# Kernel optimization log

Measured on AMD Instinct MI355X. Metric: run time of the kernel, lower is better.

## Reference

```python
import jax, jax.numpy as jnp
import numpy as np

B, T, C = 4, 2048, 1024
H = 16
HD = C // H


def setup_inputs() -> dict:
    key = jax.random.key(0)
    k1, k2, k3 = jax.random.split(key, 3)
    x = jax.random.normal(k1, (B, T, C), dtype=jnp.float32)
    w_qkv = jax.random.normal(k2, (C, 3 * C), dtype=jnp.float32) * (C ** -0.5)
    w_proj = jax.random.normal(k3, (C, C), dtype=jnp.float32) * (C ** -0.5)
    b_proj = jnp.zeros((C,), dtype=jnp.float32)
    return {"x": x, "w_qkv": w_qkv, "w_proj": w_proj, "b_proj": b_proj}


def reference(x, w_qkv, w_proj, b_proj):
    Bd, Td, Cd = x.shape
    scale = HD ** -0.5
    qkv = x @ w_qkv  # [B,T,3C]
    q, k, v = jnp.split(qkv, 3, axis=-1)
    # [B,H,T,HD]
    q = q.reshape(Bd, Td, H, HD).transpose(0, 2, 1, 3)
    k = k.reshape(Bd, Td, H, HD).transpose(0, 2, 1, 3)
    v = v.reshape(Bd, Td, H, HD).transpose(0, 2, 1, 3)
    att = jnp.einsum('bhqd,bhkd->bhqk', q, k) * scale
    causal = jnp.triu(jnp.ones((Td, Td), dtype=bool), k=1)
    att = jnp.where(causal, -jnp.inf, att)
    att = jax.nn.softmax(att, axis=-1)
    y = jnp.einsum('bhqk,bhkd->bhqd', att, v)
    y = y.transpose(0, 2, 1, 3).reshape(Bd, Td, Cd)
    return y @ w_proj + b_proj
```

## Files before the change

### kernel.cpp

```cpp
#include <hip/hip_runtime.h>

typedef unsigned short u16;
typedef __attribute__((ext_vector_type(8))) short short8;
typedef __attribute__((ext_vector_type(4))) short short4v;
typedef __attribute__((ext_vector_type(4))) float floatx4;
typedef __attribute__((ext_vector_type(4))) unsigned short ushort4v;

#define B_ 4
#define T_ 2048
#define C_ 1024
#define H_ 16
#define HD_ 64

static __device__ __forceinline__ u16 f2bf(float f) {
  union { float f; unsigned int i; } c; c.f = f;
  unsigned int u = c.i;
  return (u16)((u + 0x7FFFu + ((u >> 16) & 1u)) >> 16);
}
static __device__ __forceinline__ unsigned pk2(float lo, float hi) {
  union { float f; unsigned u; } a, b; a.f = hi; b.f = lo;
  return __builtin_amdgcn_perm(a.u, b.u, 0x07060302u);
}

static __device__ __forceinline__ void gload16(const u16* g, u16* l) {
  __builtin_amdgcn_global_load_lds(
      (const __attribute__((address_space(1))) unsigned int*)(g),
      (__attribute__((address_space(3))) unsigned int*)(l), 16, 0, 0);
}

__global__ __launch_bounds__(256) void prep_k(const float* __restrict__ x,
                                              const float* __restrict__ w_qkv,
                                              const float* __restrict__ w_proj,
                                              u16* __restrict__ xbf,
                                              u16* __restrict__ wqkvT,
                                              u16* __restrict__ wprojT) {
  const int bid = blockIdx.x;
  if (bid < 8192) {
    const int i = bid * 256 + threadIdx.x;
    const float4 f = ((const float4*)x)[i];
    ushort4v o;
    o.x = f2bf(f.x); o.y = f2bf(f.y); o.z = f2bf(f.z); o.w = f2bf(f.w);
    *(ushort4v*)(xbf + (size_t)i * 4) = o;
    return;
  }
  __shared__ u16 tile[32][33];
  const float* in;
  u16* out;
  int R, Cc, tb;
  if (bid < 11264) {
    in = w_qkv; out = wqkvT; R = C_; Cc = 3 * C_; tb = bid - 8192;
  } else {
    in = w_proj; out = wprojT; R = C_; Cc = C_; tb = bid - 11264;
  }
  const int tpr = Cc / 32;
  const int bx = (tb % tpr) * 32;
  const int by = (tb / tpr) * 32;
  const int tx = threadIdx.x & 31;
  const int ty = threadIdx.x >> 5;
  #pragma unroll
  for (int i = ty; i < 32; i += 8)
    tile[i][tx] = f2bf(in[(size_t)(by + i) * Cc + bx + tx]);
  __syncthreads();
  #pragma unroll
  for (int i = ty; i < 32; i += 8)
    out[(size_t)(bx + i) * R + by + tx] = tile[tx][i];
}

__global__ __launch_bounds__(256) void vtrans_k(const u16* __restrict__ qkv,
                                                u16* __restrict__ vt) {
  __shared__ u16 tile[64][74];
  const int tt = blockIdx.x;
  const int bh = blockIdx.y;
  const int b = bh >> 4, h = bh & 15;
  const int tid = threadIdx.x;
  const u16* src = qkv + ((size_t)b * T_ + tt * 64) * (3 * C_) + 2 * C_ + h * HD_;
  #pragma unroll
  for (int ss = tid; ss < 512; ss += 256) {
    const int row = ss >> 3, c8 = (ss & 7) * 8;
    *(short8*)(&tile[row][c8]) = *(const short8*)(src + (size_t)row * (3 * C_) + c8);
  }
  __syncthreads();
  u16* dst = vt + (size_t)bh * HD_ * T_ + tt * 64;
  #pragma unroll
  for (int ss = tid; ss < 512; ss += 256) {
    const int tc = (ss & 7) * 8, d = ss >> 3;
    short8 o;
    #pragma unroll
    for (int j = 0; j < 8; j++) o[j] = (short)tile[tc + j][d];
    *(short8*)(dst + (size_t)d * T_ + tc) = o;
  }
}

template <int MODE>
__global__ __launch_bounds__(256) void gemm_bt(const u16* __restrict__ A,
                                               const u16* __restrict__ Bt,
                                               u16* __restrict__ outb,
                                               float* __restrict__ outf,
                                               const float* __restrict__ bias,
                                               int M, int N, int K) {
  __shared__ __align__(16) u16 As[2][128 * 32];
  __shared__ __align__(16) u16 Bs[2][128 * 32];
  const int bid = blockIdx.x;
  const int s = bid >> 3;
  const int tM = ((bid & 7) * 8 + (s & 7)) * 128;
  const int tN = (s >> 3) * 128;
  const int tid = threadIdx.x;
  const int wave = tid >> 6;
  const int lane = tid & 63;
  const int lr = lane & 15;
  const int quad = lane >> 4;
  const int wm = (wave >> 1) * 64;
  const int wn = (wave & 1) * 64;

  const int srow = lane >> 2;
  const int skofs = ((lane & 3) ^ ((lane >> 3) & 3)) * 8;

  const floatx4 zf = {0.f, 0.f, 0.f, 0.f};
  floatx4 acc[4][4];
  #pragma unroll
  for (int i = 0; i < 4; i++)
    #pragma unroll
    for (int j = 0; j < 4; j++) acc[i][j] = zf;

  const int csw = (lr >> 1) & 3;

  for (int k0 = 0; k0 < K; k0 += 64) {
    __syncthreads();
    #pragma unroll
    for (int half = 0; half < 2; half++) {
      const int kk = k0 + half * 32;
      #pragma unroll
      for (int j = 0; j < 2; j++) {
        const int seg = wave * 2 + j;
        const int row = seg * 16 + srow;
        gload16(A + (size_t)(tM + row) * K + kk + skofs, &As[half][seg * 512]);
        gload16(Bt + (size_t)(tN + row) * K + kk + skofs, &Bs[half][seg * 512]);
      }
    }
    __syncthreads();

    #pragma unroll
    for (int half = 0; half < 2; half++) {
      short8 af[4], bfr[4];
      #pragma unroll
      for (int mt = 0; mt < 4; mt++)
        af[mt] = *(const short8*)(&As[half][(wm + mt * 16 + lr) * 32 + ((quad ^ csw) * 8)]);
      #pragma unroll
      for (int nt = 0; nt < 4; nt++)
        bfr[nt] = *(const short8*)(&Bs[half][(wn + nt * 16 + lr) * 32 + ((quad ^ csw) * 8)]);
      #pragma unroll
      for (int mt = 0; mt < 4; mt++)
        #pragma unroll
        for (int nt = 0; nt < 4; nt++)
          acc[mt][nt] = __builtin_amdgcn_mfma_f32_16x16x32_bf16(af[mt], bfr[nt],
                                                                acc[mt][nt], 0, 0, 0);
    }
  }

  #pragma unroll
  for (int mt = 0; mt < 4; mt++) {
    const int m0 = tM + wm + mt * 16 + quad * 4;
    #pragma unroll
    for (int nt = 0; nt < 4; nt++) {
      const int n = tN + wn + nt * 16 + lr;
      #pragma unroll
      for (int r = 0; r < 4; r++) {
        const float v = acc[mt][nt][r];
        const size_t m = (size_t)(m0 + r);
        if (MODE == 2) __builtin_nontemporal_store(v + bias[n], &outf[m * N + n]);
        else           outb[m * N + n] = f2bf(v);
      }
    }
  }
}

__global__ __launch_bounds__(256, 4) void attn_k(const u16* __restrict__ qkv,
                                                 const u16* __restrict__ vt,
                                                 u16* __restrict__ y) {
  __shared__ __align__(16) u16 Ks[64 * 64];
  __shared__ __align__(16) u16 Vs[64 * 64];
  const int bid = blockIdx.x;
  const int s = bid >> 3;
  const int qp = s >> 3;
  const int bh = ((s & 7) << 3) | (bid & 7);
  const int b = bh >> 4, h = bh & 15;
  const int tid = threadIdx.x;
  const int wave = tid >> 6;
  const int lane = tid & 63;
  const int lr = lane & 15;
  const int quad = lane >> 4;
  const int qtA = qp, qtB = 31 - qp;

  const int srow = lane >> 3;
  const int skofs = ((lane & 7) ^ ((lane >> 3) & 7)) * 8;
  const int gsw = lr & 7;

  const size_t RS = 3 * C_;
  const u16* qcol = qkv + (size_t)b * T_ * RS + h * HD_;
  const u16* kcol = qcol + C_;

  const size_t qrA = (size_t)(qtA * 64 + wave * 16 + lr) * RS;
  const size_t qrB = (size_t)(qtB * 64 + wave * 16 + lr) * RS;
  const short8 aq0A = *(const short8*)(qcol + qrA + quad * 8);
  const short8 aq1A = *(const short8*)(qcol + qrA + 32 + quad * 8);
  const short8 aq0B = *(const short8*)(qcol + qrB + quad * 8);
  const short8 aq1B = *(const short8*)(qcol + qrB + 32 + quad * 8);

  const floatx4 zf = {0.f, 0.f, 0.f, 0.f};
  const float C1 = 0.125f * 1.44269504f;
  const float C2 = -16.0f * 1.44269504f;
  const short8 vones = {16256, 16256, 16256, 16256, 16256, 16256, 16256, 16256};

  floatx4 accA[4], accB[4];
  floatx4 accSA = zf, accSB = zf;
  #pragma unroll
  for (int i = 0; i < 4; i++) { accA[i] = zf; accB[i] = zf; }

  for (int kt = 0; kt <= qtB; kt++) {
    const bool doA = (kt <= qtA);
    const bool diagA = (kt == qtA), diagB = (kt == qtB);
    __syncthreads();
    #pragma unroll
    for (int j = 0; j < 2; j++) {
      const int seg = wave * 2 + j;
      const int row = seg * 8 + srow;
      gload16(kcol + (size_t)(kt * 64 + row) * RS + skofs, &Ks[seg * 512]);
      gload16(vt + ((size_t)bh * HD_ + row) * T_ + kt * 64 + skofs, &Vs[seg * 512]);
    }
    __syncthreads();

    float peA[4][4], peB[4][4];
    #pragma unroll
    for (int nt = 0; nt < 4; nt++) {
      const short8 bk0 =
          *(const short8*)(&Ks[(nt * 16 + lr) * 64 + ((quad ^ gsw) * 8)]);
      const short8 bk1 =
          *(const short8*)(&Ks[(nt * 16 + lr) * 64 + (((quad + 4) ^ gsw) * 8)]);
      {
        floatx4 st = __builtin_amdgcn_mfma_f32_16x16x32_bf16(
            bk1, aq1B,
            __builtin_amdgcn_mfma_f32_16x16x32_bf16(bk0, aq0B, zf, 0, 0, 0),
            0, 0, 0);
        #pragma unroll
        for (int r = 0; r < 4; r++) {
          float pe = __builtin_amdgcn_exp2f(fmaf(st[r], C1, C2));
          if (diagB && (nt * 16 + quad * 4 + r > wave * 16 + lr)) pe = 0.f;
          peB[nt][r] = pe;
        }
      }
      if (doA) {
        floatx4 st = __builtin_amdgcn_mfma_f32_16x16x32_bf16(
            bk1, aq1A,
            __builtin_amdgcn_mfma_f32_16x16x32_bf16(bk0, aq0A, zf, 0, 0, 0),
            0, 0, 0);
        #pragma unroll
        for (int r = 0; r < 4; r++) {
          float pe = __builtin_amdgcn_exp2f(fmaf(st[r], C1, C2));
          if (diagA && (nt * 16 + quad * 4 + r > wave * 16 + lr)) pe = 0.f;
          peA[nt][r] = pe;
        }
      }
    }

    short8 pB[2], pA[2];
    #pragma unroll
    for (int h2 = 0; h2 < 2; h2++) {
      union { unsigned u[4]; short8 s8; } w;
      w.u[0] = pk2(peB[2 * h2][0], peB[2 * h2][1]);
      w.u[1] = pk2(peB[2 * h2][2], peB[2 * h2][3]);
      w.u[2] = pk2(peB[2 * h2 + 1][0], peB[2 * h2 + 1][1]);
      w.u[3] = pk2(peB[2 * h2 + 1][2], peB[2 * h2 + 1][3]);
      pB[h2] = w.s8;
    }
    if (doA) {
      #pragma unroll
      for (int h2 = 0; h2 < 2; h2++) {
        union { unsigned u[4]; short8 s8; } w;
        w.u[0] = pk2(peA[2 * h2][0], peA[2 * h2][1]);
        w.u[1] = pk2(peA[2 * h2][2], peA[2 * h2][3]);
        w.u[2] = pk2(peA[2 * h2 + 1][0], peA[2 * h2 + 1][1]);
        w.u[3] = pk2(peA[2 * h2 + 1][2], peA[2 * h2 + 1][3]);
        pA[h2] = w.s8;
      }
    }

    #pragma unroll
    for (int h2 = 0; h2 < 2; h2++) {
      accSB = __builtin_amdgcn_mfma_f32_16x16x32_bf16(vones, pB[h2], accSB, 0, 0, 0);
      if (doA)
        accSA = __builtin_amdgcn_mfma_f32_16x16x32_bf16(vones, pA[h2], accSA, 0, 0, 0);
      #pragma unroll
      for (int dt = 0; dt < 4; dt++) {
        const int base = (dt * 16 + lr) * 64;
        const int cl = h2 * 4 + (quad >> 1);
        const int off_lo = ((cl ^ gsw) * 8) + (quad & 1) * 4;
        const int off_hi = (((cl + 2) ^ gsw) * 8) + (quad & 1) * 4;
        const short4v vlo = *(const short4v*)(&Vs[base + off_lo]);
        const short4v vhi = *(const short4v*)(&Vs[base + off_hi]);
        const short8 av = __builtin_shufflevector(vlo, vhi, 0, 1, 2, 3, 4, 5, 6, 7);
        accB[dt] = __builtin_amdgcn_mfma_f32_16x16x32_bf16(av, pB[h2], accB[dt], 0, 0, 0);
        if (doA)
          accA[dt] = __builtin_amdgcn_mfma_f32_16x16x32_bf16(av, pA[h2], accA[dt], 0, 0, 0);
      }
    }
  }

  #pragma unroll
  for (int ph = 0; ph < 2; ph++) {
    const int qt = ph ? qtB : qtA;
    const floatx4* acc = ph ? accB : accA;
    const float inv = 1.f / (ph ? accSB[0] : accSA[0]);
    const int qg = qt * 64 + wave * 16 + lr;
    u16* yrow = y + ((size_t)(b * T_ + qg)) * C_ + h * HD_;
    #pragma unroll
    for (int dt = 0; dt < 4; dt++) {
      ushort4v o;
      #pragma unroll
      for (int r = 0; r < 4; r++) o[r] = f2bf(acc[dt][r] * inv);
      *(ushort4v*)(yrow + dt * 16 + quad * 4) = o;
    }
  }
}

extern "C" void kernel_launch(void* const* d_in, const int* in_sizes, int n_in,
                              void* d_out, int out_size, void* d_ws, size_t ws_size,
                              hipStream_t stream) {
  const float* x      = (const float*)d_in[0];
  const float* w_qkv  = (const float*)d_in[1];
  const float* w_proj = (const float*)d_in[2];
  const float* b_proj = (const float*)d_in[3];
  float* out = (float*)d_out;

  u16* ws = (u16*)d_ws;
  const size_t SZ = (size_t)B_ * T_ * C_;
  u16* xbf    = ws;
  u16* wqkvT  = xbf + SZ;
  u16* wprojT = wqkvT + (size_t)3 * C_ * C_;
  u16* qkvw   = wprojT + (size_t)C_ * C_;
  u16* vtw    = qkvw + 3 * SZ;
  u16* yw     = xbf;

  prep_k<<<12288, 256, 0, stream>>>(x, w_qkv, w_proj, xbf, wqkvT, wprojT);
  gemm_bt<1><<<1536, 256, 0, stream>>>(
      xbf, wqkvT, qkvw, nullptr, nullptr, B_ * T_, 3 * C_, C_);
  vtrans_k<<<dim3(T_ / 64, B_ * H_), 256, 0, stream>>>(qkvw, vtw);
  attn_k<<<1024, 256, 0, stream>>>(qkvw, vtw, yw);
  gemm_bt<2><<<512, 256, 0, stream>>>(
      yw, wprojT, nullptr, out, b_proj, B_ * T_, C_, C_);
}
```

Before: 246.0 us.

## Fuse V transpose into QKV GEMM epilogue via LDS staging

Removes the separate vtrans_k kernel. Output tiles of the QKV GEMM that fall in the V region are now transposed through shared memory and written straight into the [B,H,HD,T] layout. This saves one launch and a full read and write of V from global memory. In exchange, those V blocks pay extra epilogue syncs and LDS traffic, and the As/Bs buffers are merged into one LDS array so it can be reused.

```diff
diff --git a/kernel.cpp b/kernel.cpp
--- a/kernel.cpp
+++ b/kernel.cpp
@@ -20,6 +20,9 @@
 static __device__ __forceinline__ unsigned pk2(float lo, float hi) {
   union { float f; unsigned u; } a, b; a.f = hi; b.f = lo;
   return __builtin_amdgcn_perm(a.u, b.u, 0x07060302u);
+}
+static __device__ __forceinline__ unsigned pk2r(float lo, float hi) {
+  return (unsigned)f2bf(lo) | ((unsigned)f2bf(hi) << 16);
 }
 
 static __device__ __forceinline__ void gload16(const u16* g, u16* l) {
@@ -66,40 +69,15 @@
     out[(size_t)(bx + i) * R + by + tx] = tile[tx][i];
 }
 
-__global__ __launch_bounds__(256) void vtrans_k(const u16* __restrict__ qkv,
-                                                u16* __restrict__ vt) {
-  __shared__ u16 tile[64][74];
-  const int tt = blockIdx.x;
-  const int bh = blockIdx.y;
-  const int b = bh >> 4, h = bh & 15;
-  const int tid = threadIdx.x;
-  const u16* src = qkv + ((size_t)b * T_ + tt * 64) * (3 * C_) + 2 * C_ + h * HD_;
-  #pragma unroll
-  for (int ss = tid; ss < 512; ss += 256) {
-    const int row = ss >> 3, c8 = (ss & 7) * 8;
-    *(short8*)(&tile[row][c8]) = *(const short8*)(src + (size_t)row * (3 * C_) + c8);
-  }
-  __syncthreads();
-  u16* dst = vt + (size_t)bh * HD_ * T_ + tt * 64;
-  #pragma unroll
-  for (int ss = tid; ss < 512; ss += 256) {
-    const int tc = (ss & 7) * 8, d = ss >> 3;
-    short8 o;
-    #pragma unroll
-    for (int j = 0; j < 8; j++) o[j] = (short)tile[tc + j][d];
-    *(short8*)(dst + (size_t)d * T_ + tc) = o;
-  }
-}
-
 template <int MODE>
 __global__ __launch_bounds__(256) void gemm_bt(const u16* __restrict__ A,
                                                const u16* __restrict__ Bt,
                                                u16* __restrict__ outb,
+                                               u16* __restrict__ outv,
                                                float* __restrict__ outf,
                                                const float* __restrict__ bias,
                                                int M, int N, int K) {
-  __shared__ __align__(16) u16 As[2][128 * 32];
-  __shared__ __align__(16) u16 Bs[2][128 * 32];
+  __shared__ __align__(16) u16 lds[16384];
   const int bid = blockIdx.x;
   const int s = bid >> 3;
   const int tM = ((bid & 7) * 8 + (s & 7)) * 128;
@@ -133,8 +111,8 @@
       for (int j = 0; j < 2; j++) {
         const int seg = wave * 2 + j;
         const int row = seg * 16 + srow;
-        gload16(A + (size_t)(tM + row) * K + kk + skofs, &As[half][seg * 512]);
-        gload16(Bt + (size_t)(tN + row) * K + kk + skofs, &Bs[half][seg * 512]);
+        gload16(A + (size_t)(tM + row) * K + kk + skofs, &lds[half * 4096 + seg * 512]);
+        gload16(Bt + (size_t)(tN + row) * K + kk + skofs, &lds[8192 + half * 4096 + seg * 512]);
       }
     }
     __syncthreads();
@@ -144,10 +122,10 @@
       short8 af[4], bfr[4];
       #pragma unroll
       for (int mt = 0; mt < 4; mt++)
-        af[mt] = *(const short8*)(&As[half][(wm + mt * 16 + lr) * 32 + ((quad ^ csw) * 8)]);
+        af[mt] = *(const short8*)(&lds[half * 4096 + (wm + mt * 16 + lr) * 32 + ((quad ^ csw) * 8)]);
       #pragma unroll
       for (int nt = 0; nt < 4; nt++)
-        bfr[nt] = *(const short8*)(&Bs[half][(wn + nt * 16 + lr) * 32 + ((quad ^ csw) * 8)]);
+        bfr[nt] = *(const short8*)(&lds[8192 + half * 4096 + (wn + nt * 16 + lr) * 32 + ((quad ^ csw) * 8)]);
       #pragma unroll
       for (int mt = 0; mt < 4; mt++)
         #pragma unroll
@@ -155,6 +133,39 @@
           acc[mt][nt] = __builtin_amdgcn_mfma_f32_16x16x32_bf16(af[mt], bfr[nt],
                                                                 acc[mt][nt], 0, 0, 0);
     }
+  }
+
+  if (MODE == 1 && tN >= 2 * C_) {
+    const int b = tM >> 11;
+    const int t0 = tM & (T_ - 1);
+    const int h0 = (tN - 2 * C_) >> 6;
+    #pragma unroll
+    for (int pass = 0; pass < 2; pass++) {
+      __syncthreads();
+      if ((wave & 1) == pass) {
+        #pragma unroll
+        for (int nt = 0; nt < 4; nt++) {
+          const int nr = nt * 16 + lr;
+          #pragma unroll
+          for (int mt = 0; mt < 4; mt++) {
+            const int mr = wm + mt * 16 + quad * 4;
+            *(unsigned*)(&lds[nr * 136 + mr]) = pk2r(acc[mt][nt][0], acc[mt][nt][1]);
+            *(unsigned*)(&lds[nr * 136 + mr + 2]) = pk2r(acc[mt][nt][2], acc[mt][nt][3]);
+          }
+        }
+      }
+      __syncthreads();
+      const int bh = b * H_ + h0 + pass;
+      u16* vbase = outv + (size_t)bh * HD_ * T_ + t0;
+      #pragma unroll
+      for (int i = 0; i < 4; i++) {
+        const int c = tid + i * 256;
+        const int nr = c >> 4, m8 = (c & 15) * 8;
+        const short8 v = *(const short8*)(&lds[nr * 136 + m8]);
+        *(short8*)(vbase + (size_t)nr * T_ + m8) = v;
+      }
+    }
+    return;
   }
 
   #pragma unroll
@@ -342,9 +353,8 @@
 
   prep_k<<<12288, 256, 0, stream>>>(x, w_qkv, w_proj, xbf, wqkvT, wprojT);
   gemm_bt<1><<<1536, 256, 0, stream>>>(
-      xbf, wqkvT, qkvw, nullptr, nullptr, B_ * T_, 3 * C_, C_);
-  vtrans_k<<<dim3(T_ / 64, B_ * H_), 256, 0, stream>>>(qkvw, vtw);
+      xbf, wqkvT, qkvw, vtw, nullptr, nullptr, B_ * T_, 3 * C_, C_);
   attn_k<<<1024, 256, 0, stream>>>(qkvw, vtw, yw);
   gemm_bt<2><<<512, 256, 0, stream>>>(
-      yw, wprojT, nullptr, out, b_proj, B_ * T_, C_, C_);
-}
+      yw, wprojT, nullptr, nullptr, out, b_proj, B_ * T_, C_, C_);
+}
```

Result: faster. 240.2 us (-2.3%).
